# Kernel optimization log

Measured on AMD Instinct MI355X. Metric: run time of the kernel, lower is better.

The kernel has to match this reference:

```python
import jax, jax.numpy as jnp
import numpy as np

MODEL_BATCHES = 2048
NUM_POINTS = 8192
N_FUNCS = 8
REMOVE_ITERS = 51  # remove_points = 51 * model_batches -> first 51 iterations dropped


def setup_inputs() -> dict:
    key = jax.random.key(0)
    k1, k2, k3, k4, k5 = jax.random.split(key, 5)
    point = jax.random.normal(k1, (MODEL_BATCHES, 2, 1), dtype=jnp.float32) * 0.1
    optimized_weights = jax.random.normal(k2, (N_FUNCS, 2, 2), dtype=jnp.float32) * 0.5
    optimized_biases = jax.random.normal(k3, (N_FUNCS, 2, 1), dtype=jnp.float32) * 0.5
    optimized_function_ops = jax.random.uniform(k4, (N_FUNCS,), dtype=jnp.float32)
    index = jax.random.randint(k5, (MODEL_BATCHES, NUM_POINTS), 0, N_FUNCS, dtype=jnp.int32)
    return {
        "point": point,
        "optimized_weights": optimized_weights,
        "optimized_biases": optimized_biases,
        "optimized_function_ops": optimized_function_ops,
        "index": index,
    }


def reference(point, optimized_weights, optimized_biases, optimized_function_ops, index):
    mb = point.shape[0]

    def step(p, idx):  # p: [mb,2,1], idx: [mb]
        W = optimized_weights[idx]          # [mb,2,2]
        b = optimized_biases[idx]           # [mb,2,1]
        op = optimized_function_ops[idx]    # [mb]
        p_new = jnp.einsum('bij,bjk->bik', W, p) + b  # [mb,2,1]
        out = jnp.concatenate([p_new[:, :, 0], op[:, None]], axis=1)  # [mb,3]
        return p_new, out

    # scan over iterations: index.T is [num_points, mb]
    _, outs = jax.lax.scan(step, point, index.T)  # outs: [num_points, mb, 3]
    pts = outs.reshape(-1, 3)  # matches torch.cat along dim 0 then squeeze
    return pts[REMOVE_ITERS * mb:, :]
```

## Files before the change

kernel.cpp:

```cpp
#include <hip/hip_runtime.h>

#define MB   2048
#define NP   8192
#define NF   8
#define RM   51
#define NCH  64
#define CH   128
#define SEG  32
#define NSEG 4


__global__ __launch_bounds__(256) void ifs_phase1(
    const int* __restrict__ idxg, const float* __restrict__ W,
    const float* __restrict__ B, float4* __restrict__ maps)
{
    __shared__ int tile[256][SEG + 1];
    __shared__ __align__(16) float tbl[NF][8];
    const int tid = threadIdx.x;
    if (tid < NF) {
        tbl[tid][0] = W[tid*4+0]; tbl[tid][1] = W[tid*4+1];
        tbl[tid][2] = W[tid*4+2]; tbl[tid][3] = W[tid*4+3];
        tbl[tid][4] = B[tid*2+0]; tbl[tid][5] = B[tid*2+1];
        tbl[tid][6] = 0.f;        tbl[tid][7] = 0.f;
    }
    const int c  = blockIdx.x >> 3;
    const int b0 = (blockIdx.x & 7) << 8;
    const int x4 = tid & 7, yy = tid >> 3;

    float a00 = 1.f, a01 = 0.f, a10 = 0.f, a11 = 1.f, c0 = 0.f, c1 = 0.f;

    for (int seg = 0; seg < NSEG; ++seg) {
        const int tb = c * CH + seg * SEG;
        #pragma unroll
        for (int p = 0; p < 8; ++p) {
            const int row = yy + p * 32;
            const int4 v = *(const int4*)(idxg + (size_t)(b0 + row) * NP + tb + x4 * 4);
            tile[row][x4*4+0] = v.x; tile[row][x4*4+1] = v.y;
            tile[row][x4*4+2] = v.z; tile[row][x4*4+3] = v.w;
        }
        __syncthreads();
        #pragma unroll
        for (int s = 0; s < SEG; ++s) {
            const int f = tile[tid][s];
            const float4 wl = *(const float4*)&tbl[f][0];
            const float4 wh = *(const float4*)&tbl[f][4];
            const float na00 = wl.x*a00 + wl.y*a10;
            const float na01 = wl.x*a01 + wl.y*a11;
            const float na10 = wl.z*a00 + wl.w*a10;
            const float na11 = wl.z*a01 + wl.w*a11;
            const float nc0  = wl.x*c0  + wl.y*c1 + wh.x;
            const float nc1  = wl.z*c0  + wl.w*c1 + wh.y;
            a00 = na00; a01 = na01; a10 = na10; a11 = na11; c0 = nc0; c1 = nc1;
        }
        __syncthreads();
    }
    const size_t n = ((size_t)c * MB + b0 + tid) * 2;
    maps[n]     = make_float4(a00, a01, a10, a11);
    maps[n + 1] = make_float4(c0,  c1,  0.f, 0.f);
}

__global__ __launch_bounds__(64) void ifs_phase2(
    const float2* __restrict__ point, const float4* __restrict__ maps,
    float2* __restrict__ pe)
{
    const int b = blockIdx.x * 64 + threadIdx.x;
    float2 p = point[b];
    float4 lo = maps[(size_t)b * 2];
    float4 hi = maps[(size_t)b * 2 + 1];
    for (int c = 0; c < NCH; ++c) {
        float4 nlo = lo, nhi = hi;
        if (c + 1 < NCH) {
            nlo = maps[((size_t)(c + 1) * MB + b) * 2];
            nhi = maps[((size_t)(c + 1) * MB + b) * 2 + 1];
        }
        pe[(size_t)c * MB + b] = p;
        const float np0 = lo.x * p.x + lo.y * p.y + hi.x;
        const float np1 = lo.z * p.x + lo.w * p.y + hi.y;
        p.x = np0; p.y = np1;
        lo = nlo; hi = nhi;
    }
}

__global__ __launch_bounds__(256) void ifs_phase3(
    const int* __restrict__ idxg, const float* __restrict__ W,
    const float* __restrict__ B, const float* __restrict__ OPS,
    const float2* __restrict__ pe, float* __restrict__ out)
{
    __shared__ int tile[256][SEG + 1];
    __shared__ __align__(16) float tbl[NF][8];
    const int tid = threadIdx.x;
    if (tid < NF) {
        tbl[tid][0] = W[tid*4+0]; tbl[tid][1] = W[tid*4+1];
        tbl[tid][2] = W[tid*4+2]; tbl[tid][3] = W[tid*4+3];
        tbl[tid][4] = B[tid*2+0]; tbl[tid][5] = B[tid*2+1];
        tbl[tid][6] = OPS[tid];   tbl[tid][7] = 0.f;
    }
    const int c  = blockIdx.x >> 3;
    const int b0 = (blockIdx.x & 7) << 8;
    const int b  = b0 + tid;
    const int x4 = tid & 7, yy = tid >> 3;

    float2 p = pe[(size_t)c * MB + b];

    for (int seg = 0; seg < NSEG; ++seg) {
        const int tb = c * CH + seg * SEG;
        #pragma unroll
        for (int p8 = 0; p8 < 8; ++p8) {
            const int row = yy + p8 * 32;
            const int4 v = *(const int4*)(idxg + (size_t)(b0 + row) * NP + tb + x4 * 4);
            tile[row][x4*4+0] = v.x; tile[row][x4*4+1] = v.y;
            tile[row][x4*4+2] = v.z; tile[row][x4*4+3] = v.w;
        }
        __syncthreads();
        #pragma unroll
        for (int s = 0; s < SEG; ++s) {
            const int f = tile[tid][s];
            const float4 wl = *(const float4*)&tbl[f][0];
            const float4 wh = *(const float4*)&tbl[f][4];
            const float np0 = wl.x * p.x + wl.y * p.y + wh.x;
            const float np1 = wl.z * p.x + wl.w * p.y + wh.y;
            p.x = np0; p.y = np1;
            const int t = c * CH + seg * SEG + s;
            if (t >= RM) {
                float* o = out + ((size_t)(t - RM) * MB + b) * 3;
                o[0] = p.x; o[1] = p.y; o[2] = wh.z;
            }
        }
        __syncthreads();
    }
}

extern "C" void kernel_launch(void* const* d_in, const int* in_sizes, int n_in,
                              void* d_out, int out_size, void* d_ws, size_t ws_size,
                              hipStream_t stream) {
    const float* point = (const float*)d_in[0];
    const float* W     = (const float*)d_in[1];
    const float* B     = (const float*)d_in[2];
    const float* OPS   = (const float*)d_in[3];
    const int*   idx   = (const int*)  d_in[4];
    float*       out   = (float*)d_out;

    float*  ws   = (float*)d_ws;
    float4* maps = (float4*)ws;
    float2* pe   = (float2*)(ws + (size_t)NCH * MB * 8);

    ifs_phase1<<<NCH * (MB / 256), 256, 0, stream>>>(idx, W, B, maps);
    ifs_phase2<<<MB / 64, 64, 0, stream>>>((const float2*)point, maps, pe);
    ifs_phase3<<<NCH * (MB / 256), 256, 0, stream>>>(idx, W, B, OPS, pe, out);
}
```

Before: 73.21 us.

## Pair-compose affine maps, load indices directly to registers, batch phase-2 map loads

```diff
diff --git a/kernel.cpp b/kernel.cpp
--- a/kernel.cpp
+++ b/kernel.cpp
@@ -9,75 +9,130 @@
 #define SEG  32
 #define NSEG 4
 
+#define ELEM(v, s) ( (((s) & 3) == 0) ? (v)[(s) >> 2].x \
+                   : (((s) & 3) == 1) ? (v)[(s) >> 2].y \
+                   : (((s) & 3) == 2) ? (v)[(s) >> 2].z \
+                   :                    (v)[(s) >> 2].w )
+
 
 __global__ __launch_bounds__(256) void ifs_phase1(
     const int* __restrict__ idxg, const float* __restrict__ W,
     const float* __restrict__ B, float4* __restrict__ maps)
 {
-    __shared__ int tile[256][SEG + 1];
-    __shared__ __align__(16) float tbl[NF][8];
+    __shared__ __align__(16) float4 pA[64];
+    __shared__ __align__(16) float2 pC[64];
     const int tid = threadIdx.x;
-    if (tid < NF) {
-        tbl[tid][0] = W[tid*4+0]; tbl[tid][1] = W[tid*4+1];
-        tbl[tid][2] = W[tid*4+2]; tbl[tid][3] = W[tid*4+3];
-        tbl[tid][4] = B[tid*2+0]; tbl[tid][5] = B[tid*2+1];
-        tbl[tid][6] = 0.f;        tbl[tid][7] = 0.f;
+    if (tid < 64) {
+        const int fb = tid & 7;
+        const int fa = tid >> 3;
+        const float wa00 = W[fa*4+0], wa01 = W[fa*4+1], wa10 = W[fa*4+2], wa11 = W[fa*4+3];
+        const float wb00 = W[fb*4+0], wb01 = W[fb*4+1], wb10 = W[fb*4+2], wb11 = W[fb*4+3];
+        const float ba0 = B[fa*2+0], ba1 = B[fa*2+1];
+        const float bb0 = B[fb*2+0], bb1 = B[fb*2+1];
+        pA[tid] = make_float4(wa00*wb00 + wa01*wb10, wa00*wb01 + wa01*wb11,
+                              wa10*wb00 + wa11*wb10, wa10*wb01 + wa11*wb11);
+        pC[tid] = make_float2(wa00*bb0 + wa01*bb1 + ba0,
+                              wa10*bb0 + wa11*bb1 + ba1);
     }
-    const int c  = blockIdx.x >> 3;
-    const int b0 = (blockIdx.x & 7) << 8;
-    const int x4 = tid & 7, yy = tid >> 3;
+    __syncthreads();
+
+    const int c = blockIdx.x >> 3;
+    const int b = ((blockIdx.x & 7) << 8) + tid;
+    const int4* ip = (const int4*)(idxg + (size_t)b * NP + c * CH);
+
+    int4 va[8], vb[8];
+    #pragma unroll
+    for (int k = 0; k < 8; ++k) va[k] = ip[k];
 
     float a00 = 1.f, a01 = 0.f, a10 = 0.f, a11 = 1.f, c0 = 0.f, c1 = 0.f;
 
     for (int seg = 0; seg < NSEG; ++seg) {
-        const int tb = c * CH + seg * SEG;
+        if (seg + 1 < NSEG) {
+            #pragma unroll
+            for (int k = 0; k < 8; ++k) vb[k] = ip[(seg + 1) * 8 + k];
+        }
         #pragma unroll
-        for (int p = 0; p < 8; ++p) {
-            const int row = yy + p * 32;
-            const int4 v = *(const int4*)(idxg + (size_t)(b0 + row) * NP + tb + x4 * 4);
-            tile[row][x4*4+0] = v.x; tile[row][x4*4+1] = v.y;
-            tile[row][x4*4+2] = v.z; tile[row][x4*4+3] = v.w;
-        }
-        __syncthreads();
-        #pragma unroll
-        for (int s = 0; s < SEG; ++s) {
-            const int f = tile[tid][s];
-            const float4 wl = *(const float4*)&tbl[f][0];
-            const float4 wh = *(const float4*)&tbl[f][4];
-            const float na00 = wl.x*a00 + wl.y*a10;
-            const float na01 = wl.x*a01 + wl.y*a11;
-            const float na10 = wl.z*a00 + wl.w*a10;
-            const float na11 = wl.z*a01 + wl.w*a11;
-            const float nc0  = wl.x*c0  + wl.y*c1 + wh.x;
-            const float nc1  = wl.z*c0  + wl.w*c1 + wh.y;
+        for (int s = 0; s < SEG; s += 2) {
+            const int e = ELEM(va, s + 1) * 8 + ELEM(va, s);
+            const float4 P = pA[e];
+            const float2 q = pC[e];
+            const float na00 = P.x*a00 + P.y*a10;
+            const float na01 = P.x*a01 + P.y*a11;
+            const float na10 = P.z*a00 + P.w*a10;
+            const float na11 = P.z*a01 + P.w*a11;
+            const float nc0  = P.x*c0  + P.y*c1 + q.x;
+            const float nc1  = P.z*c0  + P.w*c1 + q.y;
             a00 = na00; a01 = na01; a10 = na10; a11 = na11; c0 = nc0; c1 = nc1;
         }
-        __syncthreads();
+        #pragma unroll
+        for (int k = 0; k < 8; ++k) va[k] = vb[k];
     }
-    const size_t n = ((size_t)c * MB + b0 + tid) * 2;
+    const size_t n = ((size_t)c * MB + b) * 2;
     maps[n]     = make_float4(a00, a01, a10, a11);
     maps[n + 1] = make_float4(c0,  c1,  0.f, 0.f);
 }
 
-__global__ __launch_bounds__(64) void ifs_phase2(
+__global__ __launch_bounds__(256) void ifs_phase2(
     const float2* __restrict__ point, const float4* __restrict__ maps,
     float2* __restrict__ pe)
 {
-    const int b = blockIdx.x * 64 + threadIdx.x;
+    const int b = blockIdx.x * 256 + threadIdx.x;
     float2 p = point[b];
-    float4 lo = maps[(size_t)b * 2];
-    float4 hi = maps[(size_t)b * 2 + 1];
-    for (int c = 0; c < NCH; ++c) {
-        float4 nlo = lo, nhi = hi;
-        if (c + 1 < NCH) {
-            nlo = maps[((size_t)(c + 1) * MB + b) * 2];
-            nhi = maps[((size_t)(c + 1) * MB + b) * 2 + 1];
+    float4 lo[8], hi[8], nlo[8], nhi[8];
+    #pragma unroll
+    for (int k = 0; k < 8; ++k) {
+        lo[k] = maps[((size_t)k * MB + b) * 2];
+        hi[k] = maps[((size_t)k * MB + b) * 2 + 1];
+    }
+    for (int g = 0; g < 8; ++g) {
+        if (g < 7) {
+            #pragma unroll
+            for (int k = 0; k < 8; ++k) {
+                nlo[k] = maps[((size_t)((g + 1) * 8 + k) * MB + b) * 2];
+                nhi[k] = maps[((size_t)((g + 1) * 8 + k) * MB + b) * 2 + 1];
+            }
         }
-        pe[(size_t)c * MB + b] = p;
-        const float np0 = lo.x * p.x + lo.y * p.y + hi.x;
-        const float np1 = lo.z * p.x + lo.w * p.y + hi.y;
-        p.x = np0; p.y = np1;
-        lo = nlo; hi = nhi;
+        #pragma unroll
+        for (int k = 0; k < 8; ++k) {
+            pe[(size_t)(g * 8 + k) * MB + b] = p;
+            const float nx = lo[k].x * p.x + lo[k].y * p.y + hi[k].x;
+            const float ny = lo[k].z * p.x + lo[k].w * p.y + hi[k].y;
+            p.x = nx; p.y = ny;
+        }
+        #pragma unroll
+        for (int k = 0; k < 8; ++k) { lo[k] = nlo[k]; hi[k] = nhi[k]; }
+    }
+}
+
+template <bool CHECK>
+__device__ __forceinline__ void phase3_body(
+    const int4* ip, const float4* tA, const float4* tB,
+    float2 p, float* o, int c)
+{
+    int4 va[8], vb[8];
+    #pragma unroll
+    for (int k = 0; k < 8; ++k) va[k] = ip[k];
+
+    for (int seg = 0; seg < NSEG; ++seg) {
+        if (seg + 1 < NSEG) {
+            #pragma unroll
+            for (int k = 0; k < 8; ++k) vb[k] = ip[(seg + 1) * 8 + k];
+        }
+        #pragma unroll
+        for (int s = 0; s < SEG; ++s) {
+            const int f = ELEM(va, s);
+            const float4 w  = tA[f];
+            const float4 bb = tB[f];
+            const float nx = w.x * p.x + w.y * p.y + bb.x;
+            const float ny = w.z * p.x + w.w * p.y + bb.y;
+            p.x = nx; p.y = ny;
+            if (!CHECK || (seg * SEG + s) >= RM) {
+                o[0] = p.x; o[1] = p.y; o[2] = bb.z;
+            }
+            o += MB * 3;
+        }
+        #pragma unroll
+        for (int k = 0; k < 8; ++k) va[k] = vb[k];
     }
 }
 
@@ -86,48 +141,24 @@
     const float* __restrict__ B, const float* __restrict__ OPS,
     const float2* __restrict__ pe, float* __restrict__ out)
 {
-    __shared__ int tile[256][SEG + 1];
-    __shared__ __align__(16) float tbl[NF][8];
+    __shared__ __align__(16) float4 tA[NF];
+    __shared__ __align__(16) float4 tB[NF];
     const int tid = threadIdx.x;
     if (tid < NF) {
-        tbl[tid][0] = W[tid*4+0]; tbl[tid][1] = W[tid*4+1];
-        tbl[tid][2] = W[tid*4+2]; tbl[tid][3] = W[tid*4+3];
-        tbl[tid][4] = B[tid*2+0]; tbl[tid][5] = B[tid*2+1];
-        tbl[tid][6] = OPS[tid];   tbl[tid][7] = 0.f;
+        tA[tid] = make_float4(W[tid*4+0], W[tid*4+1], W[tid*4+2], W[tid*4+3]);
+        tB[tid] = make_float4(B[tid*2+0], B[tid*2+1], OPS[tid], 0.f);
     }
-    const int c  = blockIdx.x >> 3;
-    const int b0 = (blockIdx.x & 7) << 8;
-    const int b  = b0 + tid;
-    const int x4 = tid & 7, yy = tid >> 3;
+    __syncthreads();
 
-    float2 p = pe[(size_t)c * MB + b];
+    const int c = blockIdx.x >> 3;
+    const int b = ((blockIdx.x & 7) << 8) + tid;
+    const int4* ip = (const int4*)(idxg + (size_t)b * NP + c * CH);
 
-    for (int seg = 0; seg < NSEG; ++seg) {
-        const int tb = c * CH + seg * SEG;
-        #pragma unroll
-        for (int p8 = 0; p8 < 8; ++p8) {
-            const int row = yy + p8 * 32;
-            const int4 v = *(const int4*)(idxg + (size_t)(b0 + row) * NP + tb + x4 * 4);
-            tile[row][x4*4+0] = v.x; tile[row][x4*4+1] = v.y;
-            tile[row][x4*4+2] = v.z; tile[row][x4*4+3] = v.w;
-        }
-        __syncthreads();
-        #pragma unroll
-        for (int s = 0; s < SEG; ++s) {
-            const int f = tile[tid][s];
-            const float4 wl = *(const float4*)&tbl[f][0];
-            const float4 wh = *(const float4*)&tbl[f][4];
-            const float np0 = wl.x * p.x + wl.y * p.y + wh.x;
-            const float np1 = wl.z * p.x + wl.w * p.y + wh.y;
-            p.x = np0; p.y = np1;
-            const int t = c * CH + seg * SEG + s;
-            if (t >= RM) {
-                float* o = out + ((size_t)(t - RM) * MB + b) * 3;
-                o[0] = p.x; o[1] = p.y; o[2] = wh.z;
-            }
-        }
-        __syncthreads();
-    }
+    const float2 p = pe[(size_t)c * MB + b];
+    float* o = out + ((long long)c * CH - RM) * (MB * 3) + (long long)b * 3;
+
+    if (c == 0) phase3_body<true >(ip, tA, tB, p, o, c);
+    else        phase3_body<false>(ip, tA, tB, p, o, c);
 }
 
 extern "C" void kernel_launch(void* const* d_in, const int* in_sizes, int n_in,
@@ -145,6 +176,6 @@
     float2* pe   = (float2*)(ws + (size_t)NCH * MB * 8);
 
     ifs_phase1<<<NCH * (MB / 256), 256, 0, stream>>>(idx, W, B, maps);
-    ifs_phase2<<<MB / 64, 64, 0, stream>>>((const float2*)point, maps, pe);
+    ifs_phase2<<<MB / 256, 256, 0, stream>>>((const float2*)point, maps, pe);
     ifs_phase3<<<NCH * (MB / 256), 256, 0, stream>>>(idx, W, B, OPS, pe, out);
 }
```

Measured after the change: 77.99 us. 1.07x slower.

## Stage phase3 outputs in shared memory for coalesced nontemporal vector stores

Applied to the files above, without the earlier changes.

```diff
diff --git a/kernel.cpp b/kernel.cpp
--- a/kernel.cpp
+++ b/kernel.cpp
@@ -6,15 +6,15 @@
 #define RM   51
 #define NCH  64
 #define CH   128
-#define SEG  32
-#define NSEG 4
+
+typedef float f32x4 __attribute__((ext_vector_type(4)));
 
 
 __global__ __launch_bounds__(256) void ifs_phase1(
     const int* __restrict__ idxg, const float* __restrict__ W,
     const float* __restrict__ B, float4* __restrict__ maps)
 {
-    __shared__ int tile[256][SEG + 1];
+    __shared__ int tile[256][33];
     __shared__ __align__(16) float tbl[NF][8];
     const int tid = threadIdx.x;
     if (tid < NF) {
@@ -29,8 +29,8 @@
 
     float a00 = 1.f, a01 = 0.f, a10 = 0.f, a11 = 1.f, c0 = 0.f, c1 = 0.f;
 
-    for (int seg = 0; seg < NSEG; ++seg) {
-        const int tb = c * CH + seg * SEG;
+    for (int seg = 0; seg < 4; ++seg) {
+        const int tb = c * CH + seg * 32;
         #pragma unroll
         for (int p = 0; p < 8; ++p) {
             const int row = yy + p * 32;
@@ -40,7 +40,7 @@
         }
         __syncthreads();
         #pragma unroll
-        for (int s = 0; s < SEG; ++s) {
+        for (int s = 0; s < 32; ++s) {
             const int f = tile[tid][s];
             const float4 wl = *(const float4*)&tbl[f][0];
             const float4 wh = *(const float4*)&tbl[f][4];
@@ -65,69 +65,116 @@
 {
     const int b = blockIdx.x * 64 + threadIdx.x;
     float2 p = point[b];
-    float4 lo = maps[(size_t)b * 2];
-    float4 hi = maps[(size_t)b * 2 + 1];
-    for (int c = 0; c < NCH; ++c) {
-        float4 nlo = lo, nhi = hi;
-        if (c + 1 < NCH) {
-            nlo = maps[((size_t)(c + 1) * MB + b) * 2];
-            nhi = maps[((size_t)(c + 1) * MB + b) * 2 + 1];
+    float4 lo[8], hi[8], nlo[8], nhi[8];
+    #pragma unroll
+    for (int k = 0; k < 8; ++k) {
+        lo[k] = maps[((size_t)k * MB + b) * 2];
+        hi[k] = maps[((size_t)k * MB + b) * 2 + 1];
+    }
+    for (int g = 0; g < 8; ++g) {
+        if (g < 7) {
+            #pragma unroll
+            for (int k = 0; k < 8; ++k) {
+                nlo[k] = maps[((size_t)((g + 1) * 8 + k) * MB + b) * 2];
+                nhi[k] = maps[((size_t)((g + 1) * 8 + k) * MB + b) * 2 + 1];
+            }
         }
-        pe[(size_t)c * MB + b] = p;
-        const float np0 = lo.x * p.x + lo.y * p.y + hi.x;
-        const float np1 = lo.z * p.x + lo.w * p.y + hi.y;
-        p.x = np0; p.y = np1;
-        lo = nlo; hi = nhi;
+        #pragma unroll
+        for (int k = 0; k < 8; ++k) {
+            pe[(size_t)(g * 8 + k) * MB + b] = p;
+            const float nx = lo[k].x * p.x + lo[k].y * p.y + hi[k].x;
+            const float ny = lo[k].z * p.x + lo[k].w * p.y + hi[k].y;
+            p.x = nx; p.y = ny;
+        }
+        #pragma unroll
+        for (int k = 0; k < 8; ++k) { lo[k] = nlo[k]; hi[k] = nhi[k]; }
     }
 }
 
+template <bool CHECK>
+__device__ __forceinline__ void phase3_body(
+    const int* __restrict__ idxg, const float4* tA, const float4* tB,
+    float (*sbuf)[4][256][3], int (*tile)[36],
+    int c, int b0, int tid, const float2* __restrict__ pe,
+    float* __restrict__ out)
+{
+    const int x4 = tid & 7, yy = tid >> 3;
+    float2 p = pe[(size_t)c * MB + b0 + tid];
+
+    int s_[3], r_[3];
+    #pragma unroll
+    for (int k = 0; k < 3; ++k) {
+        const int w = 4 * (tid + 256 * k);
+        s_[k] = w / 768;
+        r_[k] = w - s_[k] * 768;
+    }
+    long long off[3];
+    #pragma unroll
+    for (int k = 0; k < 3; ++k)
+        off[k] = (long long)(c * CH + s_[k] - RM) * (MB * 3) + b0 * 3 + r_[k];
+
+    int gg = 0;
+    for (int seg = 0; seg < 4; ++seg) {
+        const int tb = c * CH + seg * 32;
+        #pragma unroll
+        for (int p8 = 0; p8 < 8; ++p8) {
+            const int row = yy + p8 * 32;
+            *(int4*)&tile[row][x4*4] = *(const int4*)(idxg + (size_t)(b0 + row) * NP + tb + x4 * 4);
+        }
+        __syncthreads();
+        #pragma unroll
+        for (int g = 0; g < 8; ++g, ++gg) {
+            const int buf = gg & 1;
+            const int4 f4 = *(const int4*)&tile[tid][g*4];
+            const int fs[4] = {f4.x, f4.y, f4.z, f4.w};
+            #pragma unroll
+            for (int s = 0; s < 4; ++s) {
+                const float4 w  = tA[fs[s]];
+                const float4 bb = tB[fs[s]];
+                const float nx = w.x * p.x + w.y * p.y + bb.x;
+                const float ny = w.z * p.x + w.w * p.y + bb.y;
+                p.x = nx; p.y = ny;
+                sbuf[buf][s][tid][0] = p.x;
+                sbuf[buf][s][tid][1] = p.y;
+                sbuf[buf][s][tid][2] = bb.z;
+            }
+            __syncthreads();
+            const int t0 = seg * 32 + g * 4;
+            const float* flat = &sbuf[buf][0][0][0];
+            #pragma unroll
+            for (int k = 0; k < 3; ++k) {
+                if (!CHECK || (t0 + s_[k]) >= RM) {
+                    const f32x4 v = *(const f32x4*)(flat + 4 * (tid + 256 * k));
+                    __builtin_nontemporal_store(v, (f32x4*)(out + off[k]));
+                }
+                off[k] += 4LL * (MB * 3);
+            }
+        }
+        __syncthreads();
+    }
+}
+
+template <bool DUMMY>
 __global__ __launch_bounds__(256) void ifs_phase3(
     const int* __restrict__ idxg, const float* __restrict__ W,
     const float* __restrict__ B, const float* __restrict__ OPS,
     const float2* __restrict__ pe, float* __restrict__ out)
 {
-    __shared__ int tile[256][SEG + 1];
-    __shared__ __align__(16) float tbl[NF][8];
+    __shared__ int tile[256][36];
+    __shared__ __align__(16) float sbuf[2][4][256][3];
+    __shared__ __align__(16) float4 tA[NF];
+    __shared__ __align__(16) float4 tB[NF];
     const int tid = threadIdx.x;
     if (tid < NF) {
-        tbl[tid][0] = W[tid*4+0]; tbl[tid][1] = W[tid*4+1];
-        tbl[tid][2] = W[tid*4+2]; tbl[tid][3] = W[tid*4+3];
-        tbl[tid][4] = B[tid*2+0]; tbl[tid][5] = B[tid*2+1];
-        tbl[tid][6] = OPS[tid];   tbl[tid][7] = 0.f;
+        tA[tid] = make_float4(W[tid*4+0], W[tid*4+1], W[tid*4+2], W[tid*4+3]);
+        tB[tid] = make_float4(B[tid*2+0], B[tid*2+1], OPS[tid], 0.f);
     }
+
     const int c  = blockIdx.x >> 3;
     const int b0 = (blockIdx.x & 7) << 8;
-    const int b  = b0 + tid;
-    const int x4 = tid & 7, yy = tid >> 3;
 
-    float2 p = pe[(size_t)c * MB + b];
-
-    for (int seg = 0; seg < NSEG; ++seg) {
-        const int tb = c * CH + seg * SEG;
-        #pragma unroll
-        for (int p8 = 0; p8 < 8; ++p8) {
-            const int row = yy + p8 * 32;
-            const int4 v = *(const int4*)(idxg + (size_t)(b0 + row) * NP + tb + x4 * 4);
-            tile[row][x4*4+0] = v.x; tile[row][x4*4+1] = v.y;
-            tile[row][x4*4+2] = v.z; tile[row][x4*4+3] = v.w;
-        }
-        __syncthreads();
-        #pragma unroll
-        for (int s = 0; s < SEG; ++s) {
-            const int f = tile[tid][s];
-            const float4 wl = *(const float4*)&tbl[f][0];
-            const float4 wh = *(const float4*)&tbl[f][4];
-            const float np0 = wl.x * p.x + wl.y * p.y + wh.x;
-            const float np1 = wl.z * p.x + wl.w * p.y + wh.y;
-            p.x = np0; p.y = np1;
-            const int t = c * CH + seg * SEG + s;
-            if (t >= RM) {
-                float* o = out + ((size_t)(t - RM) * MB + b) * 3;
-                o[0] = p.x; o[1] = p.y; o[2] = wh.z;
-            }
-        }
-        __syncthreads();
-    }
+    if (c == 0) phase3_body<true >(idxg, tA, tB, sbuf, tile, c, b0, tid, pe, out);
+    else        phase3_body<false>(idxg, tA, tB, sbuf, tile, c, b0, tid, pe, out);
 }
 
 extern "C" void kernel_launch(void* const* d_in, const int* in_sizes, int n_in,
@@ -146,5 +193,5 @@
 
     ifs_phase1<<<NCH * (MB / 256), 256, 0, stream>>>(idx, W, B, maps);
     ifs_phase2<<<MB / 64, 64, 0, stream>>>((const float2*)point, maps, pe);
-    ifs_phase3<<<NCH * (MB / 256), 256, 0, stream>>>(idx, W, B, OPS, pe, out);
+    ifs_phase3<false><<<NCH * (MB / 256), 256, 0, stream>>>(idx, W, B, OPS, pe, out);
 }
```

New measurement: 70.78 us. -3.3%, faster.
